# Optimization experiments

Hardware: AMD Instinct MI355X
Metric: run time of the kernel (lower is better)

## Reference

```python
import jax, jax.numpy as jnp
import numpy as np

B = 8192       # n_cells per batch
G = 512        # n_genes
D = 64         # expression latent dim


def setup_inputs() -> dict:
    key = jax.random.key(0)
    k1, k2 = jax.random.split(key)
    velocity = jax.random.normal(k1, (B, G), dtype=jnp.float32)
    expression_latent = jax.random.normal(k2, (B, D), dtype=jnp.float32)
    return {"velocity": velocity, "expression_latent": expression_latent}


def reference(velocity, expression_latent):
    # weighted_diff[i, j] = sum_g (v_i[g] - v_j[g])^2
    # computed via the Gram trick: ||v_i||^2 + ||v_j||^2 - 2 v_i . v_j
    # (same math as materializing the (B, B, G) diff tensor and summing over g)
    sq_norm = jnp.sum(velocity * velocity, axis=1)              # [B]
    gram = jnp.einsum('ig,jg->ij', velocity, velocity)          # [B, B]
    weighted_diff = sq_norm[:, None] + sq_norm[None, :] - 2.0 * gram  # [B, B]

    # row-softmax of latent similarity matrix
    sim_logits = jnp.einsum('id,jd->ij', expression_latent, expression_latent)  # [B, B]
    expression_similarity = jax.nn.softmax(sim_logits, axis=1)

    batch_size = velocity.shape[0]
    tangent_loss = jnp.sum(expression_similarity * weighted_diff) / (batch_size * batch_size)
    return tangent_loss
```

## Files before the change

### kernel.cpp

```cpp
#include <hip/hip_runtime.h>


#define SEL_T 32.0f

typedef _Float16 half8 __attribute__((ext_vector_type(8)));
typedef float    f32x4 __attribute__((ext_vector_type(4)));
typedef long     l2t   __attribute__((ext_vector_type(2)));

#define MFMA16(a, b, c) __builtin_amdgcn_mfma_f32_16x16x32_f16(a, b, c, 0, 0, 0)
#define MFMA8(a, b, c)  __builtin_amdgcn_mfma_f32_16x16x32_fp8_fp8(a, b, c, 0, 0, 0)

__global__ __launch_bounds__(256) void k_prep(
    const float* __restrict__ V, const float* __restrict__ E,
    float* __restrict__ n, float* __restrict__ ne,
    float* __restrict__ Z, float* __restrict__ num,
    unsigned char* __restrict__ VF8, _Float16* __restrict__ EFh,
    unsigned* __restrict__ cnt) {
    int rt = blockIdx.x;
    int tid = threadIdx.x, wave = tid >> 6, lane = tid & 63;
    if (rt == 0 && tid == 0) *cnt = 0;
    int m = lane >> 2, q = lane & 3;
    int row = rt * 16 + m;
    const float* vr = V + (size_t)row * 512;
    float sn = 0.f;
#pragma unroll
    for (int it = 0; it < 2; ++it) {
        int c = wave + it * 4;
        const float4* p0 = (const float4*)(vr + c * 64 + q * 8);
        const float4* p1 = (const float4*)(vr + c * 64 + 32 + q * 8);
        float4 a0 = p0[0], a1 = p0[1], b0 = p1[0], b1 = p1[1];
        int w0 = 0, w1 = 0, w2 = 0, w3 = 0;
        w0 = __builtin_amdgcn_cvt_pk_fp8_f32(a0.x, a0.y, w0, false);
        w0 = __builtin_amdgcn_cvt_pk_fp8_f32(a0.z, a0.w, w0, true);
        w1 = __builtin_amdgcn_cvt_pk_fp8_f32(a1.x, a1.y, w1, false);
        w1 = __builtin_amdgcn_cvt_pk_fp8_f32(a1.z, a1.w, w1, true);
        w2 = __builtin_amdgcn_cvt_pk_fp8_f32(b0.x, b0.y, w2, false);
        w2 = __builtin_amdgcn_cvt_pk_fp8_f32(b0.z, b0.w, w2, true);
        w3 = __builtin_amdgcn_cvt_pk_fp8_f32(b1.x, b1.y, w3, false);
        w3 = __builtin_amdgcn_cvt_pk_fp8_f32(b1.z, b1.w, w3, true);
        uint4 o;
        o.x = (unsigned)w0; o.y = (unsigned)w1;
        o.z = (unsigned)w2; o.w = (unsigned)w3;
        *(uint4*)(VF8 + (((size_t)rt * 8 + c) << 10) + lane * 16) = o;
        sn += a0.x*a0.x + a0.y*a0.y + a0.z*a0.z + a0.w*a0.w
            + a1.x*a1.x + a1.y*a1.y + a1.z*a1.z + a1.w*a1.w
            + b0.x*b0.x + b0.y*b0.y + b0.z*b0.z + b0.w*b0.w
            + b1.x*b1.x + b1.y*b1.y + b1.z*b1.z + b1.w*b1.w;
    }
    __shared__ float sred[4][64];
    sred[wave][lane] = sn;
    __syncthreads();
    if (tid < 16) {
        float s = 0.f;
#pragma unroll
        for (int w = 0; w < 4; ++w)
#pragma unroll
            for (int qq = 0; qq < 4; ++qq) s += sred[w][tid * 4 + qq];
        int rr = rt * 16 + tid;
        n[rr] = s;
        Z[rr] = 1.0f;
        num[rr] = 0.0f;
    }
    if (tid < 128) {
        int rl = tid >> 3, u = tid & 7;
        int erow = rt * 16 + rl;
        const float4* er = (const float4*)(E + (size_t)erow * 64);
        float4 x0 = er[u * 2], x1 = er[u * 2 + 1];
        float xf[8] = {x0.x, x0.y, x0.z, x0.w, x1.x, x1.y, x1.z, x1.w};
        half8 h;
        float se = 0.f;
#pragma unroll
        for (int k = 0; k < 8; ++k) {
            h[k] = (_Float16)xf[k];
            se += xf[k] * xf[k];
        }
        int kc = u >> 2, qq = u & 3;
        *(half8*)(EFh + ((size_t)rt * 2 + kc) * 512 + rl * 32 + qq * 8) = h;
        se += __shfl_xor(se, 1, 64);
        se += __shfl_xor(se, 2, 64);
        se += __shfl_xor(se, 4, 64);
        if (u == 0) ne[erow] = se;
    }
}

__global__ __launch_bounds__(256, 3) void k_mega(
    const unsigned char* __restrict__ VF8, const _Float16* __restrict__ EFh,
    const float* __restrict__ ne, const float* __restrict__ nrm,
    float* __restrict__ Z, float* __restrict__ num) {
    int blk0 = blockIdx.x;
    int blk = (blk0 & 7) * 260 + (blk0 >> 3);
    int by = (int)((sqrtf(8.f * (float)blk + 1.f) - 1.f) * 0.5f);
    while ((by + 1) * (by + 2) / 2 <= blk) ++by;
    while (by * (by + 1) / 2 > blk) --by;
    int bx = blk - by * (by + 1) / 2;
    int i0 = bx << 7, j0 = by << 7;
    bool diag = (bx == by);

    __shared__ float sNeI[128], sNeJ[128], sNI[128], sNJ[128];
    __shared__ float scr[1024];

    int tid = threadIdx.x;
    if (tid < 128) { sNeI[tid] = ne[i0 + tid]; sNI[tid] = nrm[i0 + tid]; }
    else { sNeJ[tid - 128] = ne[j0 + tid - 128]; sNJ[tid - 128] = nrm[j0 + tid - 128]; }
    __syncthreads();

    int wave = tid >> 6, lane = tid & 63;
    int m = lane & 15, quad = lane >> 4;
    int wi = wave & 1, wj = wave >> 1;
    int rtA = (i0 >> 4) + wi * 4;
    int rtB = (j0 >> 4) + wj * 4;
    size_t loH = (size_t)(m * 32 + quad * 8);
    size_t loB = (size_t)(m * 64 + quad * 16);

    f32x4 gacc[4][4] = {};
    for (int c = 0; c < 8; ++c) {
        l2t a[4], b[4];
#pragma unroll
        for (int im = 0; im < 4; ++im)
            a[im] = *(const l2t*)(VF8 + (((size_t)(rtA + im) * 8 + c) << 10) + loB);
#pragma unroll
        for (int jn = 0; jn < 4; ++jn)
            b[jn] = *(const l2t*)(VF8 + (((size_t)(rtB + jn) * 8 + c) << 10) + loB);
#pragma unroll
        for (int jn = 0; jn < 4; ++jn)
#pragma unroll
            for (int im = 0; im < 4; ++im) {
                gacc[im][jn] = MFMA8(a[im][0], b[jn][0], gacc[im][jn]);
                gacc[im][jn] = MFMA8(a[im][1], b[jn][1], gacc[im][jn]);
            }
    }

    half8 bh[4][2];
#pragma unroll
    for (int jn = 0; jn < 4; ++jn) {
        size_t bb = (size_t)(rtB + jn) * 2 * 512 + loH;
        bh[jn][0] = *(const half8*)(EFh + bb);
        bh[jn][1] = *(const half8*)(EFh + bb + 512);
    }
    float zj[4] = {}, nj_[4] = {};
#pragma unroll
    for (int im = 0; im < 4; ++im) {
        size_t ab = (size_t)(rtA + im) * 2 * 512 + loH;
        half8 ah0 = *(const half8*)(EFh + ab);
        half8 ah1 = *(const half8*)(EFh + ab + 512);
        f32x4 zi4 = {0.f, 0.f, 0.f, 0.f};
        f32x4 ni4 = {0.f, 0.f, 0.f, 0.f};
#pragma unroll
        for (int jn = 0; jn < 4; ++jn) {
            f32x4 acc = {0.f, 0.f, 0.f, 0.f};
            acc = MFMA16(ah0, bh[jn][0], acc);
            acc = MFMA16(ah1, bh[jn][1], acc);
            int jl = (wj << 6) + jn * 16 + m;
            int jg = j0 + jl;
            float nej = sNeJ[jl], nnj = sNJ[jl];
            f32x4 g4 = gacc[im][jn];
            bool p[4];
            bool anyp = false;
#pragma unroll
            for (int r = 0; r < 4; ++r) {
                int il = (wi << 6) + im * 16 + quad * 4 + r;
                int ig = i0 + il;
                float nei = sNeI[il];
                p[r] = (acc[r] > fminf(nei, nej) - SEL_T) && (!diag || ig < jg);
                anyp |= p[r];
            }
            if (__builtin_amdgcn_ballot_w64(anyp)) {
#pragma unroll
                for (int r = 0; r < 4; ++r) {
                    if (p[r]) {
                        int il = (wi << 6) + im * 16 + quad * 4 + r;
                        float nei = sNeI[il], nni = sNI[il];
                        float s = acc[r];
                        float wiw = __expf(s - nei);
                        float wjw = __expf(s - nej);
                        float wd = nni + nnj - 2.f * g4[r];
                        zi4[r] += wiw;  ni4[r] += wiw * wd;
                        zj[jn] += wjw;  nj_[jn] += wjw * wd;
                    }
                }
            }
        }
#pragma unroll
        for (int msk = 1; msk < 16; msk <<= 1) {
#pragma unroll
            for (int r = 0; r < 4; ++r) {
                zi4[r] += __shfl_xor(zi4[r], msk, 64);
                ni4[r] += __shfl_xor(ni4[r], msk, 64);
            }
        }
        if (m == 0) {
            int row0 = (wi << 6) + im * 16 + quad * 4;
            *(f32x4*)(scr + (wj << 7) + row0)       = zi4;
            *(f32x4*)(scr + 256 + (wj << 7) + row0) = ni4;
        }
    }
#pragma unroll
    for (int msk = 16; msk < 64; msk <<= 1) {
#pragma unroll
        for (int jn = 0; jn < 4; ++jn) {
            zj[jn]  += __shfl_xor(zj[jn],  msk, 64);
            nj_[jn] += __shfl_xor(nj_[jn], msk, 64);
        }
    }
    if (quad == 0) {
#pragma unroll
        for (int jn = 0; jn < 4; ++jn) {
            int jl = (wj << 6) + jn * 16 + m;
            scr[512 + (wi << 7) + jl] = zj[jn];
            scr[768 + (wi << 7) + jl] = nj_[jn];
        }
    }
    __syncthreads();
    if (tid < 128) {
        float az = scr[tid]       + scr[128 + tid];
        float an = scr[256 + tid] + scr[384 + tid];
        if (az != 0.f || an != 0.f) {
            atomicAdd(Z + i0 + tid,   az);
            atomicAdd(num + i0 + tid, an);
        }
    } else {
        int cidx = tid - 128;
        float az = scr[512 + cidx] + scr[640 + cidx];
        float an = scr[768 + cidx] + scr[896 + cidx];
        if (az != 0.f || an != 0.f) {
            atomicAdd(Z + j0 + cidx,   az);
            atomicAdd(num + j0 + cidx, an);
        }
    }
}

__global__ __launch_bounds__(256) void k_red(
    const float* __restrict__ Z, const float* __restrict__ num,
    double* __restrict__ part, unsigned* __restrict__ cnt,
    float* __restrict__ out) {
    int r = (blockIdx.x << 8) + threadIdx.x;
    __shared__ double sd[256];
    sd[threadIdx.x] = (double)num[r] / (double)Z[r];
    __syncthreads();
    for (int st = 128; st > 0; st >>= 1) {
        if (threadIdx.x < st) sd[threadIdx.x] += sd[threadIdx.x + st];
        __syncthreads();
    }
    if (threadIdx.x == 0) {
        part[blockIdx.x] = sd[0];
        __threadfence();
        unsigned old = atomicAdd(cnt, 1u);
        if (old == 31u) {
            __threadfence();
            double a = 0.0;
            for (int k = 0; k < 32; ++k) a += part[k];
            out[0] = (float)(a / 67108864.0);
        }
    }
}

extern "C" void kernel_launch(void* const* d_in, const int* in_sizes, int n_in,
                              void* d_out, int out_size, void* d_ws, size_t ws_size,
                              hipStream_t stream) {
    const float* V = (const float*)d_in[0];
    const float* E = (const float*)d_in[1];
    float* out = (float*)d_out;
    char* ws = (char*)d_ws;

    float*         n_   = (float*)(ws + 0);
    float*         ne   = (float*)(ws + 32768);
    float*         Z    = (float*)(ws + 65536);
    float*         num  = (float*)(ws + 98304);
    unsigned char* VF8  = (unsigned char*)(ws + 131072);
    _Float16*      EFh  = (_Float16*)(ws + 4325376);
    double*        part = (double*)(ws + 5373952);
    unsigned*      cnt  = (unsigned*)(ws + 5374208);

    k_prep<<<512, 256, 0, stream>>>(V, E, n_, ne, Z, num, VF8, EFh, cnt);
    k_mega<<<2080, 256, 0, stream>>>(VF8, EFh, ne, n_, Z, num);
    k_red <<<32, 256, 0, stream>>>(Z, num, part, cnt, out);
}
```

Before: 135.1 us.

## Fuse final reduction into main kernel via last-block counter, raise occupancy

Removes the separate reduction kernel: each main-kernel block increments a global counter after its atomics, and the last block reads Z and num (via atomic reads) and performs the full 8192-row reduction itself. This saves one kernel launch and its gap. It also raises launch bounds from 3 to 4 blocks per CU and loads the half-precision B fragments inside the loop instead of preloading them, to cut register pressure. The tradeoff is a serialized tail, where one block does the whole final reduction, plus a possible increase in global loads.

```diff
diff --git a/kernel.cpp b/kernel.cpp
--- a/kernel.cpp
+++ b/kernel.cpp
@@ -83,10 +83,11 @@
     }
 }
 
-__global__ __launch_bounds__(256, 3) void k_mega(
+__global__ __launch_bounds__(256, 4) void k_mega(
     const unsigned char* __restrict__ VF8, const _Float16* __restrict__ EFh,
     const float* __restrict__ ne, const float* __restrict__ nrm,
-    float* __restrict__ Z, float* __restrict__ num) {
+    float* __restrict__ Z, float* __restrict__ num,
+    unsigned* __restrict__ cnt, float* __restrict__ out) {
     int blk0 = blockIdx.x;
     int blk = (blk0 & 7) * 260 + (blk0 >> 3);
     int by = (int)((sqrtf(8.f * (float)blk + 1.f) - 1.f) * 0.5f);
@@ -97,7 +98,8 @@
     bool diag = (bx == by);
 
     __shared__ float sNeI[128], sNeJ[128], sNI[128], sNJ[128];
-    __shared__ float scr[1024];
+    __shared__ __align__(16) float scr[1024];
+    __shared__ unsigned lastFlag;
 
     int tid = threadIdx.x;
     if (tid < 128) { sNeI[tid] = ne[i0 + tid]; sNI[tid] = nrm[i0 + tid]; }
@@ -130,13 +132,6 @@
             }
     }
 
-    half8 bh[4][2];
-#pragma unroll
-    for (int jn = 0; jn < 4; ++jn) {
-        size_t bb = (size_t)(rtB + jn) * 2 * 512 + loH;
-        bh[jn][0] = *(const half8*)(EFh + bb);
-        bh[jn][1] = *(const half8*)(EFh + bb + 512);
-    }
     float zj[4] = {}, nj_[4] = {};
 #pragma unroll
     for (int im = 0; im < 4; ++im) {
@@ -147,9 +142,12 @@
         f32x4 ni4 = {0.f, 0.f, 0.f, 0.f};
 #pragma unroll
         for (int jn = 0; jn < 4; ++jn) {
+            size_t bb = (size_t)(rtB + jn) * 2 * 512 + loH;
+            half8 bh0 = *(const half8*)(EFh + bb);
+            half8 bh1 = *(const half8*)(EFh + bb + 512);
             f32x4 acc = {0.f, 0.f, 0.f, 0.f};
-            acc = MFMA16(ah0, bh[jn][0], acc);
-            acc = MFMA16(ah1, bh[jn][1], acc);
+            acc = MFMA16(ah0, bh0, acc);
+            acc = MFMA16(ah1, bh1, acc);
             int jl = (wj << 6) + jn * 16 + m;
             int jg = j0 + jl;
             float nej = sNeJ[jl], nnj = sNJ[jl];
@@ -227,30 +225,31 @@
             atomicAdd(num + j0 + cidx, an);
         }
     }
-}
-
-__global__ __launch_bounds__(256) void k_red(
-    const float* __restrict__ Z, const float* __restrict__ num,
-    double* __restrict__ part, unsigned* __restrict__ cnt,
-    float* __restrict__ out) {
-    int r = (blockIdx.x << 8) + threadIdx.x;
-    __shared__ double sd[256];
-    sd[threadIdx.x] = (double)num[r] / (double)Z[r];
-    __syncthreads();
-    for (int st = 128; st > 0; st >>= 1) {
-        if (threadIdx.x < st) sd[threadIdx.x] += sd[threadIdx.x + st];
-        __syncthreads();
-    }
-    if (threadIdx.x == 0) {
-        part[blockIdx.x] = sd[0];
+
+    __syncthreads();
+    if (tid == 0) {
         __threadfence();
         unsigned old = atomicAdd(cnt, 1u);
-        if (old == 31u) {
-            __threadfence();
-            double a = 0.0;
-            for (int k = 0; k < 32; ++k) a += part[k];
-            out[0] = (float)(a / 67108864.0);
-        }
+        lastFlag = (old == 2079u) ? 1u : 0u;
+    }
+    __syncthreads();
+    if (lastFlag) {
+        double acc = 0.0;
+#pragma unroll
+        for (int k = 0; k < 32; ++k) {
+            int r = (k << 8) + tid;
+            float z  = atomicAdd(Z + r, 0.0f);
+            float nv = atomicAdd(num + r, 0.0f);
+            acc += (double)nv / (double)z;
+        }
+        double* sd = (double*)scr;
+        sd[tid] = acc;
+        __syncthreads();
+        for (int st = 128; st > 0; st >>= 1) {
+            if (tid < st) sd[tid] += sd[tid + st];
+            __syncthreads();
+        }
+        if (tid == 0) out[0] = (float)(sd[0] / 67108864.0);
     }
 }
 
@@ -268,10 +267,8 @@
     float*         num  = (float*)(ws + 98304);
     unsigned char* VF8  = (unsigned char*)(ws + 131072);
     _Float16*      EFh  = (_Float16*)(ws + 4325376);
-    double*        part = (double*)(ws + 5373952);
-    unsigned*      cnt  = (unsigned*)(ws + 5374208);
+    unsigned*      cnt  = (unsigned*)(ws + 5373952);
 
     k_prep<<<512, 256, 0, stream>>>(V, E, n_, ne, Z, num, VF8, EFh, cnt);
-    k_mega<<<2080, 256, 0, stream>>>(VF8, EFh, ne, n_, Z, num);
-    k_red <<<32, 256, 0, stream>>>(Z, num, part, cnt, out);
+    k_mega<<<2080, 256, 0, stream>>>(VF8, EFh, ne, n_, Z, num, cnt, out);
 }
```

New measurement: 208.6 us. +54.4%, slower.
